# Kernel optimization log

Hardware: AMD Instinct MI355X
Metric: run time of the kernel (lower is better)

## Reference

```python
import jax, jax.numpy as jnp
import numpy as np

EPS = 1e-16


def setup_inputs() -> dict:
    key = jax.random.key(0)
    k1, k2 = jax.random.split(key)
    p = jax.random.normal(k1, (2, 32, 2048, 4), dtype=jnp.float32)
    q = jax.random.normal(k2, (32, 2048, 4), dtype=jnp.float32)
    return {"p": p, "q": q}


def reference(p, q):
    # im=False path: take the real part of the complex generated momenta
    p_real = p[0]                      # (B, N, 4)
    # loss_norm_choice='p3', take_sqrt=True: use 3-momenta (drop energy)
    p3 = p_real[..., 1:]               # (B, N, 3)
    q3 = q[..., 1:]                    # (B, M, 3)
    # Pairwise Euclidean distance (cdist) via the expanded quadratic form to
    # avoid materializing the (B, N, M, 3) difference tensor.
    x2 = jnp.sum(p3 * p3, axis=-1)     # (B, N)
    y2 = jnp.sum(q3 * q3, axis=-1)     # (B, M)
    xy = jnp.einsum('bnd,bmd->bnm', p3, q3)  # (B, N, M)
    dist_sq = x2[..., :, None] + y2[..., None, :] - 2.0 * xy
    dist = jnp.sqrt(jnp.maximum(dist_sq, 0.0) + EPS)  # (B, N, M)
    # Bidirectional nearest-neighbor min-reduction
    min_pq = jnp.min(dist, axis=-1)    # (B, N)
    min_qp = jnp.min(dist, axis=-2)    # (B, M)
    chamfer_loss = jnp.sum((min_pq + min_qp) * 0.5)
    return chamfer_loss
```

## Files before the change

### kernel.cpp

```cpp
#include <hip/hip_runtime.h>
#include <math.h>


#define NPTS   2048
#define NBATCH 32
#define NTOT   (2 * NBATCH * NPTS)
#define EPSF   1e-16f
#define BIGF   3.4e38f

__device__ __forceinline__ float min3f(float a, float b, float c) {
    return fminf(fminf(a, b), c);
}

__global__ __launch_bounds__(256) void chamfer_tile_kernel(
    const float* __restrict__ P, const float* __restrict__ Q,
    unsigned int* __restrict__ ws, float* __restrict__ out)
{
    __shared__ float4 sp[256];
    __shared__ float4 sq[256];
    __shared__ float  scol[4][256];

    const int tid = threadIdx.x;
    const int tx  = tid & 15;
    const int ty  = tid >> 4;
    const int bi  = blockIdx.x;
    const int bj  = blockIdx.y;
    const int b   = blockIdx.z;

    if (bi == 0 && bj == 0 && b == 0 && tid == 0) *out = 0.f;

    {
        float4 pv = ((const float4*)P)[(size_t)b * NPTS + bi * 256 + tid];
        sp[tid] = make_float4(pv.y, pv.z, pv.w,
                              pv.y*pv.y + pv.z*pv.z + pv.w*pv.w);
        float4 qv = ((const float4*)Q)[(size_t)b * NPTS + bj * 256 + tid];
        sq[tid] = make_float4(-2.f*qv.y, -2.f*qv.z, -2.f*qv.w,
                              qv.y*qv.y + qv.z*qv.z + qv.w*qv.w);
    }
    __syncthreads();

    float px[16], py[16], pz[16], x2[16];
    #pragma unroll
    for (int k = 0; k < 16; ++k) {
        float4 v = sp[ty + 16 * k];
        px[k] = v.x; py[k] = v.y; pz[k] = v.z; x2[k] = v.w;
    }

    float rowacc[16], colacc[16];
    #pragma unroll
    for (int k = 0; k < 16; ++k) { rowacc[k] = BIGF; colacc[k] = BIGF; }

    for (int jp = 0; jp < 8; ++jp) {
        float4 q0 = sq[tx + 32 * jp];
        float4 q1 = sq[tx + 32 * jp + 16];
        float c0 = BIGF, c1 = BIGF;
        #pragma unroll
        for (int k = 0; k < 16; k += 2) {
            float t00 = fmaf(px[k],   q0.x, fmaf(py[k],   q0.y, fmaf(pz[k],   q0.z, x2[k])));
            float t01 = fmaf(px[k],   q1.x, fmaf(py[k],   q1.y, fmaf(pz[k],   q1.z, x2[k])));
            float t10 = fmaf(px[k+1], q0.x, fmaf(py[k+1], q0.y, fmaf(pz[k+1], q0.z, x2[k+1])));
            float t11 = fmaf(px[k+1], q1.x, fmaf(py[k+1], q1.y, fmaf(pz[k+1], q1.z, x2[k+1])));
            rowacc[k]   = min3f(rowacc[k],   t00 + q0.w, t01 + q1.w);
            rowacc[k+1] = min3f(rowacc[k+1], t10 + q0.w, t11 + q1.w);
            c0 = min3f(c0, t00, t10);
            c1 = min3f(c1, t01, t11);
        }
        colacc[2*jp]     = c0;
        colacc[2*jp + 1] = c1;
    }

    #pragma unroll
    for (int k = 0; k < 16; ++k) {
        float v = rowacc[k];
        v = fminf(v, __shfl_xor(v, 1));
        v = fminf(v, __shfl_xor(v, 2));
        v = fminf(v, __shfl_xor(v, 4));
        v = fminf(v, __shfl_xor(v, 8));
        rowacc[k] = v;
    }
    if (tx == 0) {
        #pragma unroll
        for (int k = 0; k < 16; ++k) {
            float d2 = fmaxf(rowacc[k], 0.f);
            atomicMin(&ws[b * NPTS + bi * 256 + (ty + 16 * k)],
                      __float_as_uint(d2));
        }
    }

    #pragma unroll
    for (int j = 0; j < 16; ++j) {
        float v = colacc[j];
        v = fminf(v, __shfl_xor(v, 16));
        v = fminf(v, __shfl_xor(v, 32));
        colacc[j] = v;
    }
    {
        const int wv   = tid >> 6;
        const int lane = tid & 63;
        if (lane < 16) {
            #pragma unroll
            for (int j = 0; j < 16; ++j) scol[wv][j * 16 + lane] = colacc[j];
        }
    }
    __syncthreads();
    {
        const int c = tid;
        float v = fminf(fminf(scol[0][c], scol[1][c]),
                        fminf(scol[2][c], scol[3][c]));
        float d2 = fmaxf(v + sq[c].w, 0.f);
        atomicMin(&ws[NBATCH * NPTS + b * NPTS + bj * 256 + c],
                  __float_as_uint(d2));
    }
}

__global__ __launch_bounds__(256) void chamfer_sum_kernel(
    const unsigned int* __restrict__ ws, float* __restrict__ out)
{
    __shared__ float rbuf[4];
    const int tid = threadIdx.x;
    const int i0  = blockIdx.x * 256 + tid;

    float s = 0.f;
    for (int i = i0; i < NTOT; i += gridDim.x * 256)
        s += sqrtf(__uint_as_float(ws[i]) + EPSF);

    #pragma unroll
    for (int off = 32; off > 0; off >>= 1) s += __shfl_down(s, off);
    if ((tid & 63) == 0) rbuf[tid >> 6] = s;
    __syncthreads();
    if (tid == 0)
        atomicAdd(out, 0.5f * ((rbuf[0] + rbuf[1]) + (rbuf[2] + rbuf[3])));
}

extern "C" void kernel_launch(void* const* d_in, const int* in_sizes, int n_in,
                              void* d_out, int out_size, void* d_ws, size_t ws_size,
                              hipStream_t stream) {
    const float* P = (const float*)d_in[0];
    const float* Q = (const float*)d_in[1];
    float* out = (float*)d_out;
    unsigned int* ws = (unsigned int*)d_ws;

    hipMemsetAsync(ws, 0x7F, (size_t)NTOT * sizeof(unsigned int), stream);

    dim3 grid(NPTS / 256, NPTS / 256, NBATCH);
    chamfer_tile_kernel<<<grid, 256, 0, stream>>>(P, Q, ws, out);

    chamfer_sum_kernel<<<128, 256, 0, stream>>>(ws, out);
}
```

Before: 80.08 us.

## Replace atomicMin reductions with per-tile partial-min writes and drop memset

Each tile block now writes its row and column partial minima to a dedicated workspace slot with plain coalesced stores, where before it did global atomicMin updates. The sum kernel then reduces the 8 partials per point before the sqrt and the sum. This removes the hipMemsetAsync launch and the atomic contention. In exchange the workspace grows to 8x, so the second kernel reads more data.

```diff
diff --git a/kernel.cpp b/kernel.cpp
--- a/kernel.cpp
+++ b/kernel.cpp
@@ -4,7 +4,8 @@
 
 #define NPTS   2048
 #define NBATCH 32
-#define NTOT   (2 * NBATCH * NPTS)
+#define NCH    8
+#define WS_SIDE_FLOATS ((size_t)NBATCH * NCH * NCH * 256)
 #define EPSF   1e-16f
 #define BIGF   3.4e38f
 
@@ -14,11 +15,12 @@
 
 __global__ __launch_bounds__(256) void chamfer_tile_kernel(
     const float* __restrict__ P, const float* __restrict__ Q,
-    unsigned int* __restrict__ ws, float* __restrict__ out)
+    float* __restrict__ ws, float* __restrict__ out)
 {
     __shared__ float4 sp[256];
     __shared__ float4 sq[256];
     __shared__ float  scol[4][256];
+    __shared__ float  rrow[256];
 
     const int tid = threadIdx.x;
     const int tx  = tid & 15;
@@ -76,15 +78,7 @@
         v = fminf(v, __shfl_xor(v, 2));
         v = fminf(v, __shfl_xor(v, 4));
         v = fminf(v, __shfl_xor(v, 8));
-        rowacc[k] = v;
-    }
-    if (tx == 0) {
-        #pragma unroll
-        for (int k = 0; k < 16; ++k) {
-            float d2 = fmaxf(rowacc[k], 0.f);
-            atomicMin(&ws[b * NPTS + bi * 256 + (ty + 16 * k)],
-                      __float_as_uint(d2));
-        }
+        if (tx == 0) rrow[ty + 16 * k] = v;
     }
 
     #pragma unroll
@@ -103,26 +97,43 @@
         }
     }
     __syncthreads();
+
     {
-        const int c = tid;
-        float v = fminf(fminf(scol[0][c], scol[1][c]),
-                        fminf(scol[2][c], scol[3][c]));
-        float d2 = fmaxf(v + sq[c].w, 0.f);
-        atomicMin(&ws[NBATCH * NPTS + b * NPTS + bj * 256 + c],
-                  __float_as_uint(d2));
+        float v = fminf(fminf(scol[0][tid], scol[1][tid]),
+                        fminf(scol[2][tid], scol[3][tid]));
+        float* wsC = ws + WS_SIDE_FLOATS;
+        wsC[(((size_t)b * NCH + bj) * NCH + bi) * 256 + tid] = v + sq[tid].w;
+        ws[(((size_t)b * NCH + bi) * NCH + bj) * 256 + tid] = rrow[tid];
     }
 }
 
 __global__ __launch_bounds__(256) void chamfer_sum_kernel(
-    const unsigned int* __restrict__ ws, float* __restrict__ out)
+    const float* __restrict__ ws, float* __restrict__ out)
 {
     __shared__ float rbuf[4];
     const int tid = threadIdx.x;
-    const int i0  = blockIdx.x * 256 + tid;
+    const int i   = blockIdx.x * 256 + tid;
+    const int b   = i >> 11;
+    const int e   = i & 2047;
+    const int ch  = e >> 8;
+    const int el  = e & 255;
 
-    float s = 0.f;
-    for (int i = i0; i < NTOT; i += gridDim.x * 256)
-        s += sqrtf(__uint_as_float(ws[i]) + EPSF);
+    float s;
+    {
+        const float* rb = ws + ((size_t)(b * NCH + ch) * NCH) * 256 + el;
+        float v = BIGF;
+        #pragma unroll
+        for (int j = 0; j < NCH; ++j) v = fminf(v, rb[j * 256]);
+        s = sqrtf(fmaxf(v, 0.f) + EPSF);
+    }
+    {
+        const float* cb = ws + WS_SIDE_FLOATS
+                        + ((size_t)(b * NCH + ch) * NCH) * 256 + el;
+        float v = BIGF;
+        #pragma unroll
+        for (int j = 0; j < NCH; ++j) v = fminf(v, cb[j * 256]);
+        s += sqrtf(fmaxf(v, 0.f) + EPSF);
+    }
 
     #pragma unroll
     for (int off = 32; off > 0; off >>= 1) s += __shfl_down(s, off);
@@ -138,12 +149,9 @@
     const float* P = (const float*)d_in[0];
     const float* Q = (const float*)d_in[1];
     float* out = (float*)d_out;
-    unsigned int* ws = (unsigned int*)d_ws;
+    float* ws  = (float*)d_ws;
 
-    hipMemsetAsync(ws, 0x7F, (size_t)NTOT * sizeof(unsigned int), stream);
-
-    dim3 grid(NPTS / 256, NPTS / 256, NBATCH);
+    dim3 grid(NCH, NCH, NBATCH);
     chamfer_tile_kernel<<<grid, 256, 0, stream>>>(P, Q, ws, out);
-
-    chamfer_sum_kernel<<<128, 256, 0, stream>>>(ws, out);
+    chamfer_sum_kernel<<<256, 256, 0, stream>>>(ws, out);
 }
```

Result: slower. 82.83 us (+3.4%).
